# Optimization experiments

Hardware: AMD Instinct MI355X
Metric: run time of the kernel (lower is better)

## Reference

```python
import jax, jax.numpy as jnp
import numpy as np

S, B, D, H = 2048, 2, 1024, 16
DK = D // H


def rotate_half(x):
    # interleaved variant: pairs (x0,x1)->(-x1,x0)
    x1 = x[..., ::2]
    x2 = x[..., 1::2]
    return jnp.stack((-x2, x1), axis=-1).reshape(x.shape)


def apply_rope(x):
    # x: [B, H, S, dk]
    b, h, s, dk = x.shape
    pos = jnp.arange(s, dtype=jnp.float32)
    inv_freq = 1.0 / (10000.0 ** (jnp.arange(0, dk, 2, dtype=jnp.float32) / dk))
    freqs = jnp.einsum('i,j->ij', pos, inv_freq)          # [S, dk/2]
    emb = jnp.concatenate((freqs, freqs), axis=-1)        # [S, dk]  (non-interleaved cos/sin, as in source)
    cos = jnp.cos(emb)[None, None, :, :]
    sin = jnp.sin(emb)[None, None, :, :]
    return x * cos + rotate_half(x) * sin


def setup_inputs() -> dict:
    key = jax.random.key(0)
    ks = jax.random.split(key, 11)
    sc = 0.02
    return {
        'query': jax.random.normal(ks[0], (S, B, D), jnp.float32),
        'key':   jax.random.normal(ks[1], (S, B, D), jnp.float32),
        'value': jax.random.normal(ks[2], (S, B, D), jnp.float32),
        'wq': jax.random.normal(ks[3], (D, D), jnp.float32) * sc,
        'bq': jax.random.normal(ks[4], (D,), jnp.float32) * sc,
        'wk': jax.random.normal(ks[5], (D, D), jnp.float32) * sc,
        'bk': jax.random.normal(ks[6], (D,), jnp.float32) * sc,
        'wv': jax.random.normal(ks[7], (D, D), jnp.float32) * sc,
        'bv': jax.random.normal(ks[8], (D,), jnp.float32) * sc,
        'wo': jax.random.normal(ks[9], (D, D), jnp.float32) * sc,
        'bo': jax.random.normal(ks[10], (D,), jnp.float32) * sc,
    }


def reference(query, key, value, wq, bq, wk, bk, wv, bv, wo, bo):
    s_q, b, _ = query.shape
    s_k = key.shape[0]

    def split_heads(x, s):
        # [S,B,D] -> [B,H,S,dk]
        return x.transpose(1, 0, 2).reshape(b, s, H, DK).transpose(0, 2, 1, 3)

    Q = split_heads(query @ wq.T + bq, s_q)
    K = split_heads(key @ wk.T + bk, s_k)
    V = split_heads(value @ wv.T + bv, s_k)

    Q = apply_rope(Q)
    K = apply_rope(K)

    scores = jnp.einsum('bhqd,bhkd->bhqk', Q, K) / jnp.sqrt(jnp.float32(DK))
    attn = jax.nn.softmax(scores, axis=-1)
    out = jnp.einsum('bhqk,bhkd->bhqd', attn, V)          # [B,H,Sq,dk]
    out = out.transpose(0, 2, 1, 3).reshape(b, s_q, D)    # [B,Sq,D]
    out = out.transpose(1, 0, 2)                          # [Sq,B,D]
    return out @ wo.T + bo
```

## Files before the change

### kernel.cpp

```cpp
#include <hip/hip_runtime.h>
#include <cstdint>
#include <cstddef>

typedef __attribute__((ext_vector_type(4))) float f32x4;
typedef __attribute__((ext_vector_type(8))) float f32x8;
typedef __attribute__((ext_vector_type(16))) float f32x16;
typedef __attribute__((ext_vector_type(8))) __bf16 bf16x8;
typedef __attribute__((ext_vector_type(4))) __bf16 bf16x4;
typedef __attribute__((ext_vector_type(2))) __bf16 bf16x2;
typedef __attribute__((ext_vector_type(4))) unsigned int u32x4;
typedef unsigned short u16;

#define S_LEN 2048
#define BATCH 2
#define DMODEL 1024
#define NHEAD 16
#define HDK 64

__device__ __forceinline__ u16 f2bf(float f) {
    uint32_t u = __float_as_uint(f);
    u += 0x7FFFu + ((u >> 16) & 1u);
    return (u16)(u >> 16);
}

__device__ __forceinline__ void gload_lds16(const void* g, void* l) {
    __builtin_amdgcn_global_load_lds(
        (const __attribute__((address_space(1))) uint32_t*)g,
        (__attribute__((address_space(3))) uint32_t*)l, 16, 0, 0);
}

__device__ __forceinline__ unsigned pk2(float a, float b) {
    bf16x2 t;
    t[0] = (__bf16)a; t[1] = (__bf16)b;
    return __builtin_bit_cast(unsigned, t);
}

__device__ __forceinline__ f32x16 z16() {
    f32x16 v = {0.f,0.f,0.f,0.f,0.f,0.f,0.f,0.f,0.f,0.f,0.f,0.f,0.f,0.f,0.f,0.f};
    return v;
}

__global__ __launch_bounds__(256) void cvt_kernel(
    const float* __restrict__ a0, const float* __restrict__ a1, const float* __restrict__ a2,
    const float* __restrict__ a3, const float* __restrict__ a4, const float* __restrict__ a5,
    const float* __restrict__ a6,
    u16* __restrict__ o0, u16* __restrict__ o1, u16* __restrict__ o2,
    u16* __restrict__ o3, u16* __restrict__ o4, u16* __restrict__ o5,
    u16* __restrict__ o6)
{
    const int by = blockIdx.y;
    const float* s;
    u16* d;
    int n;
    switch (by) {
        case 0: s = a0; d = o0; n = 4194304; break;
        case 1: s = a1; d = o1; n = 4194304; break;
        case 2: s = a2; d = o2; n = 4194304; break;
        case 3: s = a3; d = o3; n = 1048576; break;
        case 4: s = a4; d = o4; n = 1048576; break;
        case 5: s = a5; d = o5; n = 1048576; break;
        default: s = a6; d = o6; n = 1048576; break;
    }
    int idx = (blockIdx.x * 256 + threadIdx.x) * 8;
    if (idx >= n) return;
    float4 f0 = *(const float4*)(s + idx);
    float4 f1 = *(const float4*)(s + idx + 4);
    alignas(16) u16 o[8] = {f2bf(f0.x), f2bf(f0.y), f2bf(f0.z), f2bf(f0.w),
                            f2bf(f1.x), f2bf(f1.y), f2bf(f1.z), f2bf(f1.w)};
    *(u32x4*)(d + idx) = *(const u32x4*)o;
}

__global__ __launch_bounds__(512, 6) void qkv_kernel(
    const u16* __restrict__ X0, const u16* __restrict__ X1, const u16* __restrict__ X2,
    const u16* __restrict__ W0, const u16* __restrict__ W1, const u16* __restrict__ W2,
    const float* __restrict__ B0, const float* __restrict__ B1, const float* __restrict__ B2,
    u16* __restrict__ O0, u16* __restrict__ O1, u16* __restrict__ O2)
{
    __shared__ __align__(16) u16 lA[2][128 * 32];
    __shared__ __align__(16) u16 lB[2][128 * 32];
    const int tid = threadIdx.x, wid = tid >> 6, lane = tid & 63;
    const int l15 = lane & 15, l4 = lane >> 4;
    const int p = blockIdx.y * 32 + blockIdx.x;
    const int vid = (p & 7) * 96 + (p >> 3);
    const int bx = vid & 31, byv = vid >> 5;
    const int mat = byv >> 3;
    const u16* X = mat == 0 ? X0 : (mat == 1 ? X1 : X2);
    const u16* W = mat == 0 ? W0 : (mat == 1 ? W1 : W2);
    const float* bias = mat == 0 ? B0 : (mat == 1 ? B1 : B2);
    u16* O = mat == 0 ? O0 : (mat == 1 ? O1 : O2);
    const int m0 = bx * 128, n0 = (byv & 7) * 128;
    const int mw = (wid >> 1) * 32, nw = (wid & 1) * 64;

    f32x4 acc[2][4];
#pragma unroll
    for (int i = 0; i < 2; ++i)
#pragma unroll
        for (int j = 0; j < 4; ++j) acc[i][j] = (f32x4){0.f, 0.f, 0.f, 0.f};

    const int srow = tid >> 2, sg = (tid & 3) ^ (srow & 3);

#define QSTAGE(bufi, k0_) do {                                                \
        gload_lds16(X + (size_t)(m0 + srow) * 1024 + (k0_) + sg * 8,          \
                    (char*)lA + (bufi) * 8192 + (tid & ~63) * 16);            \
        gload_lds16(W + (size_t)(n0 + srow) * 1024 + (k0_) + sg * 8,          \
                    (char*)lB + (bufi) * 8192 + (tid & ~63) * 16);            \
    } while (0)

    QSTAGE(0, 0);
    for (int ks = 0; ks < 32; ++ks) {
        const int cur = ks & 1;
        if (ks < 31) {
            QSTAGE(cur ^ 1, (ks + 1) * 32);
            asm volatile("s_waitcnt vmcnt(2)" ::: "memory");
        } else {
            asm volatile("s_waitcnt vmcnt(0)" ::: "memory");
        }
        __builtin_amdgcn_s_barrier();
        const char* la = (const char*)lA + cur * 8192;
        const char* lb = (const char*)lB + cur * 8192;
        __builtin_amdgcn_s_setprio(1);
        bf16x8 af[2], bfr[4];
#pragma unroll
        for (int f = 0; f < 2; ++f) {
            int ra = mw + f * 16 + l15;
            af[f] = *(const bf16x8*)(la + ra * 64 +
                    ((l4 * 16) ^ ((ra & 3) << 4)));
        }
#pragma unroll
        for (int f = 0; f < 4; ++f) {
            int rb = nw + f * 16 + l15;
            bfr[f] = *(const bf16x8*)(lb + rb * 64 +
                    ((l4 * 16) ^ ((rb & 3) << 4)));
        }
#pragma unroll
        for (int mf = 0; mf < 2; ++mf)
#pragma unroll
            for (int nf = 0; nf < 4; ++nf)
                acc[mf][nf] = __builtin_amdgcn_mfma_f32_16x16x32_bf16(
                    af[mf], bfr[nf], acc[mf][nf], 0, 0, 0);
        __builtin_amdgcn_s_setprio(0);
        __builtin_amdgcn_s_barrier();
    }
#undef QSTAGE

#pragma unroll
    for (int mf = 0; mf < 2; ++mf) {
#pragma unroll
        for (int nf = 0; nf < 4; ++nf) {
            int gcol = n0 + nw + nf * 16 + l15;
            float bval = bias[gcol];
            int h = gcol >> 6, d = gcol & 63;
            float invf = __expf(-(float)(d & 31) * 0.2878231366f);
#pragma unroll
            for (int i = 0; i < 4; ++i) {
                int grow = m0 + mw + mf * 16 + l4 * 4 + i;
                int s = grow >> 1, b = grow & 1;
                float v = acc[mf][nf][i] + bval;
                if (mat < 2) {
                    float p2 = __shfl_xor(v, 1);
                    float th = (float)s * invf;
                    float sn, cs;
                    __sincosf(th, &sn, &cs);
                    v = (d & 1) ? fmaf(p2, sn, v * cs) : fmaf(-p2, sn, v * cs);
                    if (mat == 0) v *= 0.18033688f;
                }
                O[((size_t)(b * NHEAD + h) * S_LEN + s) * HDK + d] = f2bf(v);
            }
        }
    }
}

__global__ __launch_bounds__(256) void vtrans_kernel(const u16* __restrict__ Vr, u16* __restrict__ Vt)
{
    __shared__ __align__(16) u16 t[64][72];
    const int tid = threadIdx.x, bh = blockIdx.y, s0 = blockIdx.x * 64;
    const u16* src = Vr + (size_t)bh * S_LEN * HDK;
    u16* dst = Vt + (size_t)bh * HDK * S_LEN;
    int r = tid >> 2, cbase = (tid & 3) * 16;
#pragma unroll
    for (int j = 0; j < 2; ++j)
        *(bf16x8*)&t[r][cbase + j * 8] =
            *(const bf16x8*)(const void*)(src + (size_t)(s0 + r) * HDK + cbase + j * 8);
    __syncthreads();
    int d = tid >> 2;
#pragma unroll
    for (int j = 0; j < 2; ++j) {
        alignas(16) u16 tmp[8];
#pragma unroll
        for (int x = 0; x < 8; ++x) {
            int lp = j * 8 + x;
            int sl = (lp & 3) | ((lp & 4) << 1) | ((lp & 8) >> 1);
            tmp[x] = t[cbase + sl][d];
        }
        *(bf16x8*)(void*)(dst + (size_t)d * S_LEN + s0 + cbase + j * 8) = *(const bf16x8*)tmp;
    }
}

__global__ __launch_bounds__(512, 4) void attn_kernel(
    const u16* __restrict__ Q, const u16* __restrict__ K,
    const u16* __restrict__ V, u16* __restrict__ O)
{
    __shared__ __align__(16) char smem[65536];
    const int tid = threadIdx.x, wid = tid >> 6, lane = tid & 63;
    const int g = wid >> 2, wv = wid & 3;
    const int l31 = lane & 31, hi = lane >> 5;
    const int p = blockIdx.y * 16 + blockIdx.x;
    const int vid = (p & 7) * 64 + (p >> 3);
    const int bh = vid >> 4, b = bh >> 4, h = bh & 15;
    const int q0 = (vid & 15) * 128;
    const u16* Qb = Q + (size_t)bh * S_LEN * HDK;
    const u16* Kb = K + (size_t)bh * S_LEN * HDK;
    const u16* Vb = V + (size_t)bh * HDK * S_LEN;

    const int qrow = q0 + wv * 32 + l31;
    bf16x8 aq[4];
#pragma unroll
    for (int ks = 0; ks < 4; ++ks)
        aq[ks] = *(const bf16x8*)(const void*)(Qb + (size_t)qrow * HDK + ks * 16 + hi * 8);

    f32x16 acc0 = z16(), acc1 = z16();
    float lpart = 0.f;

    char* gbase = smem + g * 32768;
    const int gt = tid & 255;
    const int srow = gt >> 3, lg = (gt & 7) ^ (srow & 7);
    char* sK = gbase + wv * 1024;
    char* sV = gbase + 8192 + wv * 1024;
    const u16* pk0 = Kb + (size_t)(g * 1024 + srow) * HDK + lg * 8;
    const u16* pk1 = pk0 + 32 * HDK;
    const u16* pv0 = Vb + (size_t)srow * S_LEN + g * 1024 + lg * 8;
    const u16* pv1 = pv0 + (size_t)32 * S_LEN;

    const int swl = (l31 & 7) << 4;
    const char* akr[4];
    const char* avr[4];
#pragma unroll
    for (int i = 0; i < 4; ++i) {
        akr[i] = gbase + l31 * 128 + ((i * 32 + hi * 16) ^ swl);
        avr[i] = gbase + 8192 + l31 * 128 + ((i * 32 + hi * 16) ^ swl);
    }

    gload_lds16(pk0, sK);
    gload_lds16(pk1, sK + 4096);
    gload_lds16(pv0, sV);
    gload_lds16(pv1, sV + 4096);
    pk0 += 4096; pk1 += 4096; pv0 += 64; pv1 += 64;

#define TILE(CUR_, STG_) do {                                                 \
    if (STG_) {                                                               \
        gload_lds16(pk0, sK + ((CUR_) ^ 1) * 16384);                          \
        gload_lds16(pk1, sK + ((CUR_) ^ 1) * 16384 + 4096);                   \
        gload_lds16(pv0, sV + ((CUR_) ^ 1) * 16384);                          \
        gload_lds16(pv1, sV + ((CUR_) ^ 1) * 16384 + 4096);                   \
        pk0 += 4096; pk1 += 4096; pv0 += 64; pv1 += 64;                       \
        asm volatile("s_waitcnt vmcnt(4)" ::: "memory");                      \
    } else {                                                                  \
        asm volatile("s_waitcnt vmcnt(0)" ::: "memory");                      \
    }                                                                         \
    __builtin_amdgcn_s_barrier();                                             \
    f32x16 s0 = z16(), s1 = z16();                                            \
    __builtin_amdgcn_s_setprio(1);                                            \
    _Pragma("unroll")                                                         \
    for (int ks = 0; ks < 4; ++ks) {                                          \
        bf16x8 a0 = *(const bf16x8*)(akr[ks] + (CUR_) * 16384);               \
        bf16x8 a1 = *(const bf16x8*)(akr[ks] + (CUR_) * 16384 + 4096);        \
        s0 = __builtin_amdgcn_mfma_f32_32x32x16_bf16(a0, aq[ks], s0, 0, 0, 0);\
        s1 = __builtin_amdgcn_mfma_f32_32x32x16_bf16(a1, aq[ks], s1, 0, 0, 0);\
    }                                                                         \
    __builtin_amdgcn_s_setprio(0);                                            \
    _Pragma("unroll")                                                         \
    for (int i = 0; i < 16; ++i) {                                            \
        s0[i] = __builtin_amdgcn_exp2f(s0[i]);                                \
        s1[i] = __builtin_amdgcn_exp2f(s1[i]);                                \
    }                                                                         \
    {                                                                         \
        f32x16 sm_ = s0 + s1;                                                 \
        f32x8 q8_ = __builtin_shufflevector(sm_, sm_, 0,1,2,3,4,5,6,7)        \
                  + __builtin_shufflevector(sm_, sm_, 8,9,10,11,12,13,14,15); \
        f32x4 q4_ = __builtin_shufflevector(q8_, q8_, 0,1,2,3)                \
                  + __builtin_shufflevector(q8_, q8_, 4,5,6,7);               \
        lpart += (q4_[0] + q4_[1]) + (q4_[2] + q4_[3]);                       \
    }                                                                         \
    __builtin_amdgcn_s_setprio(1);                                            \
    _Pragma("unroll")                                                         \
    for (int i = 0; i < 4; ++i) {                                             \
        const f32x16* cp = (i >> 1) ? &s1 : &s0;                              \
        const int e0 = (i & 1) * 8;                                           \
        u32x4 bw;                                                             \
        bw[0] = pk2((*cp)[e0 + 0], (*cp)[e0 + 1]);                            \
        bw[1] = pk2((*cp)[e0 + 2], (*cp)[e0 + 3]);                            \
        bw[2] = pk2((*cp)[e0 + 4], (*cp)[e0 + 5]);                            \
        bw[3] = pk2((*cp)[e0 + 6], (*cp)[e0 + 7]);                            \
        bf16x8 Bf = __builtin_bit_cast(bf16x8, bw);                           \
        bf16x8 av0 = *(const bf16x8*)(avr[i] + (CUR_) * 16384);               \
        bf16x8 av1 = *(const bf16x8*)(avr[i] + (CUR_) * 16384 + 4096);        \
        acc0 = __builtin_amdgcn_mfma_f32_32x32x16_bf16(av0, Bf, acc0, 0, 0, 0);\
        acc1 = __builtin_amdgcn_mfma_f32_32x32x16_bf16(av1, Bf, acc1, 0, 0, 0);\
    }                                                                         \
    __builtin_amdgcn_s_setprio(0);                                            \
    __builtin_amdgcn_s_barrier();                                             \
} while (0)

    for (int th = 0; th < 8; ++th) {
        TILE(0, 1);
        TILE(1, (th < 7));
    }
#undef TILE

    lpart += __shfl_xor(lpart, 32);
    float* exO = (float*)smem;
    float* exL = (float*)(smem + 36864);
    const int sl = wv * 64 + lane;
    if (g == 1) {
#pragma unroll
        for (int r4 = 0; r4 < 4; ++r4) {
            f32x4 w0 = {acc0[r4 * 4 + 0], acc0[r4 * 4 + 1], acc0[r4 * 4 + 2], acc0[r4 * 4 + 3]};
            f32x4 w1 = {acc1[r4 * 4 + 0], acc1[r4 * 4 + 1], acc1[r4 * 4 + 2], acc1[r4 * 4 + 3]};
            *(f32x4*)(exO + sl * 36 + r4 * 4) = w0;
            *(f32x4*)(exO + sl * 36 + 16 + r4 * 4) = w1;
        }
        exL[sl] = lpart;
    }
    __syncthreads();
    if (g == 0) {
        float l1 = exL[sl];
        float rl = 1.0f / (lpart + l1);
        u16* obase = O + ((size_t)qrow * BATCH + b) * DMODEL + h * HDK;
#pragma unroll
        for (int db = 0; db < 2; ++db) {
#pragma unroll
            for (int r4 = 0; r4 < 4; ++r4) {
                f32x4 part = *(const f32x4*)(exO + sl * 36 + db * 16 + r4 * 4);
                bf16x4 outv;
#pragma unroll
                for (int e = 0; e < 4; ++e) {
                    float own = db ? acc1[r4 * 4 + e] : acc0[r4 * 4 + e];
                    outv[e] = (__bf16)((own + part[e]) * rl);
                }
                *(bf16x4*)(void*)(obase + db * 32 + 8 * r4 + 4 * hi) = outv;
            }
        }
    }
}

__global__ __launch_bounds__(256) void proj_kernel(
    const u16* __restrict__ A, const u16* __restrict__ W,
    const float* __restrict__ bias, float* __restrict__ out)
{
    __shared__ __align__(16) u16 lA[2][64 * 64];
    __shared__ __align__(16) u16 lB[2][128 * 64];
    const int tid = threadIdx.x, wid = tid >> 6, lane = tid & 63;
    const int l15 = lane & 15, l4 = lane >> 4;
    const int p = blockIdx.y * 8 + blockIdx.x;
    const int vid = (p & 7) * 64 + (p >> 3);
    const int m0 = (vid & 63) * 64, n0 = (vid >> 6) * 128;
    const int nw = wid * 32;

    f32x4 acc[4][2];
#pragma unroll
    for (int i = 0; i < 4; ++i)
#pragma unroll
        for (int j = 0; j < 2; ++j) acc[i][j] = (f32x4){0.f, 0.f, 0.f, 0.f};

#define PSTAGE(bufi, k0_) do {                                                \
        _Pragma("unroll")                                                     \
        for (int it = 0; it < 2; ++it) {                                      \
            int cc = it * 256 + tid;                                          \
            int row = cc >> 3, gg = (cc & 7) ^ (row & 7);                     \
            gload_lds16(A + (size_t)(m0 + row) * 1024 + (k0_) + gg * 8,       \
                        (char*)lA + (bufi) * 8192 + (cc & ~63) * 16);         \
        }                                                                     \
        _Pragma("unroll")                                                     \
        for (int it = 0; it < 4; ++it) {                                      \
            int cc = it * 256 + tid;                                          \
            int row = cc >> 3, gg = (cc & 7) ^ (row & 7);                     \
            gload_lds16(W + (size_t)(n0 + row) * 1024 + (k0_) + gg * 8,       \
                        (char*)lB + (bufi) * 16384 + (cc & ~63) * 16);        \
        }                                                                     \
    } while (0)

    PSTAGE(0, 0);
    for (int ks = 0; ks < 16; ++ks) {
        const int cur = ks & 1;
        if (ks < 15) {
            PSTAGE(cur ^ 1, (ks + 1) * 64);
            asm volatile("s_waitcnt vmcnt(6)" ::: "memory");
        } else {
            asm volatile("s_waitcnt vmcnt(0)" ::: "memory");
        }
        __builtin_amdgcn_s_barrier();
        const char* la = (const char*)lA + cur * 8192;
        const char* lb = (const char*)lB + cur * 16384;
        __builtin_amdgcn_s_setprio(1);
#pragma unroll
        for (int kk = 0; kk < 2; ++kk) {
            bf16x8 af[4], bfr[2];
#pragma unroll
            for (int f = 0; f < 4; ++f) {
                int ra = f * 16 + l15;
                af[f] = *(const bf16x8*)(la + ra * 128 +
                        ((kk * 64 + l4 * 16) ^ ((ra & 7) << 4)));
            }
#pragma unroll
            for (int f = 0; f < 2; ++f) {
                int rb = nw + f * 16 + l15;
                bfr[f] = *(const bf16x8*)(lb + rb * 128 +
                        ((kk * 64 + l4 * 16) ^ ((rb & 7) << 4)));
            }
#pragma unroll
            for (int mf = 0; mf < 4; ++mf)
#pragma unroll
                for (int nf = 0; nf < 2; ++nf)
                    acc[mf][nf] = __builtin_amdgcn_mfma_f32_16x16x32_bf16(
                        af[mf], bfr[nf], acc[mf][nf], 0, 0, 0);
        }
        __builtin_amdgcn_s_setprio(0);
        __builtin_amdgcn_s_barrier();
    }
#undef PSTAGE

#pragma unroll
    for (int mf = 0; mf < 4; ++mf) {
#pragma unroll
        for (int nf = 0; nf < 2; ++nf) {
            int gcol = n0 + nw + nf * 16 + l15;
            float bval = bias[gcol];
#pragma unroll
            for (int i = 0; i < 4; ++i) {
                int grow = m0 + mf * 16 + l4 * 4 + i;
                out[(size_t)grow * DMODEL + gcol] = acc[mf][nf][i] + bval;
            }
        }
    }
}

extern "C" void kernel_launch(void* const* d_in, const int* in_sizes, int n_in,
                              void* d_out, int out_size, void* d_ws, size_t ws_size,
                              hipStream_t stream)
{
    (void)in_sizes; (void)n_in; (void)out_size; (void)ws_size;
    const float* q  = (const float*)d_in[0];
    const float* k  = (const float*)d_in[1];
    const float* v  = (const float*)d_in[2];
    const float* wq = (const float*)d_in[3];
    const float* bq = (const float*)d_in[4];
    const float* wk = (const float*)d_in[5];
    const float* bk = (const float*)d_in[6];
    const float* wv = (const float*)d_in[7];
    const float* bv = (const float*)d_in[8];
    const float* wo = (const float*)d_in[9];
    const float* bo = (const float*)d_in[10];

    char* ws = (char*)d_ws;
    const size_t MB = 1024 * 1024;
    u16* XQ  = (u16*)(ws + 0 * MB);
    u16* XK  = (u16*)(ws + 8 * MB);
    u16* XV  = (u16*)(ws + 16 * MB);
    u16* WQb = (u16*)(ws + 24 * MB);
    u16* WKb = (u16*)(ws + 26 * MB);
    u16* WVb = (u16*)(ws + 28 * MB);
    u16* WOb = (u16*)(ws + 30 * MB);
    u16* QR  = (u16*)(ws + 32 * MB);
    u16* KR  = (u16*)(ws + 40 * MB);
    u16* VR  = (u16*)(ws + 48 * MB);
    u16* VT  = XK;
    u16* OA  = XQ;

    cvt_kernel<<<dim3(2048, 7), 256, 0, stream>>>(q, k, v, wq, wk, wv, wo,
                                                  XQ, XK, XV, WQb, WKb, WVb, WOb);
    qkv_kernel<<<dim3(32, 24), 512, 0, stream>>>(XQ, XK, XV, WQb, WKb, WVb,
                                                 bq, bk, bv, QR, KR, VR);
    vtrans_kernel<<<dim3(32, 32), 256, 0, stream>>>(VR, VT);
    attn_kernel<<<dim3(16, 32), 512, 0, stream>>>(QR, KR, VT, OA);
    proj_kernel<<<dim3(8, 64), 256, 0, stream>>>(OA, WOb, bo, (float*)d_out);
}
```

Before: 119.6 us.

## Fuse V transpose into QKV GEMM epilogue and split QK MFMA chains

The V projection epilogue now transposes its output tile through shared memory and writes V directly in the [B,H,dk,S] layout with the permuted sequence order the attention kernel expects. This removes the separate vtrans kernel launch and the round trip of the V intermediate through global memory. The attention kernel's QK^T loop is also split into two sequential loops per accumulator, which changes MFMA issue order. The cost is extra barriers and LDS traffic in the V blocks of the QKV kernel.

```diff
diff --git a/kernel.cpp b/kernel.cpp
--- a/kernel.cpp
+++ b/kernel.cpp
@@ -74,7 +74,7 @@
     const u16* __restrict__ X0, const u16* __restrict__ X1, const u16* __restrict__ X2,
     const u16* __restrict__ W0, const u16* __restrict__ W1, const u16* __restrict__ W2,
     const float* __restrict__ B0, const float* __restrict__ B1, const float* __restrict__ B2,
-    u16* __restrict__ O0, u16* __restrict__ O1, u16* __restrict__ O2)
+    u16* __restrict__ O0, u16* __restrict__ O1, u16* __restrict__ Vt)
 {
     __shared__ __align__(16) u16 lA[2][128 * 32];
     __shared__ __align__(16) u16 lB[2][128 * 32];
@@ -87,7 +87,6 @@
     const u16* X = mat == 0 ? X0 : (mat == 1 ? X1 : X2);
     const u16* W = mat == 0 ? W0 : (mat == 1 ? W1 : W2);
     const float* bias = mat == 0 ? B0 : (mat == 1 ? B1 : B2);
-    u16* O = mat == 0 ? O0 : (mat == 1 ? O1 : O2);
     const int m0 = bx * 128, n0 = (byv & 7) * 128;
     const int mw = (wid >> 1) * 32, nw = (wid & 1) * 64;
 
@@ -143,56 +142,75 @@
     }
 #undef QSTAGE
 
-#pragma unroll
-    for (int mf = 0; mf < 2; ++mf) {
-#pragma unroll
-        for (int nf = 0; nf < 4; ++nf) {
-            int gcol = n0 + nw + nf * 16 + l15;
-            float bval = bias[gcol];
-            int h = gcol >> 6, d = gcol & 63;
-            float invf = __expf(-(float)(d & 31) * 0.2878231366f);
-#pragma unroll
-            for (int i = 0; i < 4; ++i) {
-                int grow = m0 + mw + mf * 16 + l4 * 4 + i;
-                int s = grow >> 1, b = grow & 1;
-                float v = acc[mf][nf][i] + bval;
-                if (mat < 2) {
+    if (mat < 2) {
+        u16* O = mat == 0 ? O0 : O1;
+#pragma unroll
+        for (int mf = 0; mf < 2; ++mf) {
+#pragma unroll
+            for (int nf = 0; nf < 4; ++nf) {
+                int gcol = n0 + nw + nf * 16 + l15;
+                float bval = bias[gcol];
+                int h = gcol >> 6, d = gcol & 63;
+                float invf = __expf(-(float)(d & 31) * 0.2878231366f);
+#pragma unroll
+                for (int i = 0; i < 4; ++i) {
+                    int grow = m0 + mw + mf * 16 + l4 * 4 + i;
+                    int s = grow >> 1, b = grow & 1;
+                    float v = acc[mf][nf][i] + bval;
                     float p2 = __shfl_xor(v, 1);
                     float th = (float)s * invf;
                     float sn, cs;
                     __sincosf(th, &sn, &cs);
                     v = (d & 1) ? fmaf(p2, sn, v * cs) : fmaf(-p2, sn, v * cs);
                     if (mat == 0) v *= 0.18033688f;
+                    O[((size_t)(b * NHEAD + h) * S_LEN + s) * HDK + d] = f2bf(v);
                 }
-                O[((size_t)(b * NHEAD + h) * S_LEN + s) * HDK + d] = f2bf(v);
-            }
-        }
-    }
-}
-
-__global__ __launch_bounds__(256) void vtrans_kernel(const u16* __restrict__ Vr, u16* __restrict__ Vt)
-{
-    __shared__ __align__(16) u16 t[64][72];
-    const int tid = threadIdx.x, bh = blockIdx.y, s0 = blockIdx.x * 64;
-    const u16* src = Vr + (size_t)bh * S_LEN * HDK;
-    u16* dst = Vt + (size_t)bh * HDK * S_LEN;
-    int r = tid >> 2, cbase = (tid & 3) * 16;
-#pragma unroll
-    for (int j = 0; j < 2; ++j)
-        *(bf16x8*)&t[r][cbase + j * 8] =
-            *(const bf16x8*)(const void*)(src + (size_t)(s0 + r) * HDK + cbase + j * 8);
-    __syncthreads();
-    int d = tid >> 2;
-#pragma unroll
-    for (int j = 0; j < 2; ++j) {
-        alignas(16) u16 tmp[8];
-#pragma unroll
-        for (int x = 0; x < 8; ++x) {
-            int lp = j * 8 + x;
-            int sl = (lp & 3) | ((lp & 4) << 1) | ((lp & 8) >> 1);
-            tmp[x] = t[cbase + sl][d];
-        }
-        *(bf16x8*)(void*)(dst + (size_t)d * S_LEN + s0 + cbase + j * 8) = *(const bf16x8*)tmp;
+            }
+        }
+    } else {
+        u16 vout[2][4][4];
+#pragma unroll
+        for (int mf = 0; mf < 2; ++mf)
+#pragma unroll
+            for (int nf = 0; nf < 4; ++nf) {
+                float bval = bias[n0 + nw + nf * 16 + l15];
+#pragma unroll
+                for (int i = 0; i < 4; ++i)
+                    vout[mf][nf][i] = f2bf(acc[mf][nf][i] + bval);
+            }
+        u16* t = (u16*)lA;
+        const int half = wid & 1;
+        const int rd = tid >> 3, rjc = tid & 7;
+#pragma unroll
+        for (int h_ = 0; h_ < 2; ++h_) {
+            const int hh = (n0 >> 6) + h_;
+#pragma unroll
+            for (int bb = 0; bb < 2; ++bb) {
+                __syncthreads();
+                if (half == h_) {
+#pragma unroll
+                    for (int mf = 0; mf < 2; ++mf)
+#pragma unroll
+                        for (int nf = 0; nf < 4; ++nf)
+#pragma unroll
+                            for (int i2 = 0; i2 < 2; ++i2) {
+                                int i = bb + i2 * 2;
+                                int rowL = mw + mf * 16 + l4 * 4 + i;
+                                t[(rowL >> 1) * 72 + nf * 16 + l15] = vout[mf][nf][i];
+                            }
+                }
+                __syncthreads();
+                alignas(16) u16 tmp[8];
+#pragma unroll
+                for (int x = 0; x < 8; ++x) {
+                    int lp = (rjc & 1) * 8 + x;
+                    int sl = (lp & 3) | ((lp & 4) << 1) | ((lp & 8) >> 1);
+                    tmp[x] = t[((rjc >> 1) * 16 + sl) * 72 + rd];
+                }
+                *(bf16x8*)(void*)(Vt + ((size_t)(bb * NHEAD + hh) * HDK + rd) * S_LEN
+                                  + (m0 >> 1) + rjc * 8) = *(const bf16x8*)tmp;
+            }
+        }
     }
 }
 
@@ -263,8 +281,11 @@
     _Pragma("unroll")                                                         \
     for (int ks = 0; ks < 4; ++ks) {                                          \
         bf16x8 a0 = *(const bf16x8*)(akr[ks] + (CUR_) * 16384);               \
+        s0 = __builtin_amdgcn_mfma_f32_32x32x16_bf16(a0, aq[ks], s0, 0, 0, 0);\
+    }                                                                         \
+    _Pragma("unroll")                                                         \
+    for (int ks = 0; ks < 4; ++ks) {                                          \
         bf16x8 a1 = *(const bf16x8*)(akr[ks] + (CUR_) * 16384 + 4096);        \
-        s0 = __builtin_amdgcn_mfma_f32_32x32x16_bf16(a0, aq[ks], s0, 0, 0, 0);\
         s1 = __builtin_amdgcn_mfma_f32_32x32x16_bf16(a1, aq[ks], s1, 0, 0, 0);\
     }                                                                         \
     __builtin_amdgcn_s_setprio(0);                                            \
@@ -462,15 +483,13 @@
     u16* WOb = (u16*)(ws + 30 * MB);
     u16* QR  = (u16*)(ws + 32 * MB);
     u16* KR  = (u16*)(ws + 40 * MB);
-    u16* VR  = (u16*)(ws + 48 * MB);
-    u16* VT  = XK;
+    u16* VT  = (u16*)(ws + 48 * MB);
     u16* OA  = XQ;
 
     cvt_kernel<<<dim3(2048, 7), 256, 0, stream>>>(q, k, v, wq, wk, wv, wo,
                                                   XQ, XK, XV, WQb, WKb, WVb, WOb);
     qkv_kernel<<<dim3(32, 24), 512, 0, stream>>>(XQ, XK, XV, WQb, WKb, WVb,
-                                                 bq, bk, bv, QR, KR, VR);
-    vtrans_kernel<<<dim3(32, 32), 256, 0, stream>>>(VR, VT);
+                                                 bq, bk, bv, QR, KR, VT);
     attn_kernel<<<dim3(16, 32), 512, 0, stream>>>(QR, KR, VT, OA);
     proj_kernel<<<dim3(8, 64), 256, 0, stream>>>(OA, WOb, bo, (float*)d_out);
 }
```

After: 114.5 us. -4.3%, faster.
